# Performance work log

Measured on AMD Instinct MI355X. Metric: run time of the kernel, lower is better.

Reference implementation:

```python
import jax, jax.numpy as jnp
import numpy as np

B, N, D = 32, 2048, 16
PCD = 2        # point_cloud_dimensions
K_NN = 16      # k nearest neighbours
FILTERS = 64


def setup_inputs() -> dict:
    key = jax.random.key(0)
    k1, k2, k3 = jax.random.split(key, 3)
    x = jax.random.normal(k1, (B, N, D), dtype=jnp.float32)
    # 1x1 Conv2D == dense over the last (channel) dim: W [D, FILTERS], b [FILTERS]
    W = jax.random.normal(k2, (D, FILTERS), dtype=jnp.float32) * (1.0 / np.sqrt(D))
    b = jnp.zeros((FILTERS,), dtype=jnp.float32)
    return {"x": x, "W": W, "b": b}


def reference(x, W, b):
    # points = first PCD channels; features = full input (dynamic_coordinates=True)
    points = x[:, :, :PCD]                                   # [B,N,PCD]
    # squared pairwise distances: ||p_i||^2 + ||p_j||^2 - 2 p_i.p_j  -> [B,N,N]
    sq = jnp.sum(points * points, axis=-1)                   # [B,N]
    dist = sq[:, :, None] + sq[:, None, :] - 2.0 * jnp.einsum(
        'bnd,bmd->bnm', points, points)
    # k nearest neighbours (smallest distance) per point -> [B,N,k]
    _, idx = jax.lax.top_k(-dist, K_NN)
    # gather neighbour features: [B,N,k,D]
    neigh = jax.vmap(lambda f, i: f[i])(x, idx)
    centre = x[:, :, None, :]                                # [B,N,1,D]
    # NOTE: source concatenates along the neighbour axis -> [B,N,k+1,D]
    edges = jnp.concatenate([centre, neigh - centre], axis=2)
    # 1x1 conv (linear activation) over channel dim: [B,N,k+1,FILTERS]
    conv = jnp.einsum('bnkd,df->bnkf', edges, W) + b
    # Max pooling over neighbour axis: [B,N,FILTERS]
    pooled = jnp.max(conv, axis=2)
    # shortcut_input_features=True: concat original features
    return jnp.concatenate([pooled, x], axis=-1)             # [B,N,FILTERS+D]
```

## Files before the change

kernel.cpp:

```cpp
#include <hip/hip_runtime.h>


#define B_  32
#define N_  2048
#define D_  16
#define F_  64
#define K_  16
#define OUTD (F_ + D_)
#define NQ  64
#define NS  4
#define SPLIT (N_ / NS)

__global__ __launch_bounds__(256) void proj_kernel(const float* __restrict__ x,
                                                   const float* __restrict__ W,
                                                   float* __restrict__ Y) {
    __shared__ float Ws[D_ * F_];
    __shared__ float xs[16][D_];
    const int t = threadIdx.x;
    for (int i = t; i < D_ * F_; i += 256) Ws[i] = W[i];
    const int p0 = blockIdx.x * 16;
    ((float*)xs)[t] = x[(size_t)p0 * D_ + t];
    __syncthreads();
    const int w = t >> 6, f = t & 63;
#pragma unroll
    for (int i = 0; i < 4; i++) {
        const int pw = w * 4 + i;
        float acc = 0.f;
#pragma unroll
        for (int d = 0; d < D_; d++) acc = fmaf(xs[pw][d], Ws[d * F_ + f], acc);
        Y[(size_t)(p0 + pw) * F_ + f] = acc;
    }
}

__global__ __launch_bounds__(256, 4) void knn_kernel(const float* __restrict__ x,
                                                     const float* __restrict__ bias,
                                                     const float* __restrict__ Y,
                                                     float* __restrict__ out) {
    __shared__ float2 pts[N_];
    __shared__ float  sqs[N_];
    __shared__ float  arr_raw[NS - 1][NQ * 17];
    __shared__ float  Tq[NQ];
    __shared__ int    cnt[NQ];
    __shared__ int    tiecnt[NS][NQ];
    unsigned short (*tiebuf)[NQ][K_] =
        (unsigned short (*)[NQ][K_])&arr_raw[0][0];
    int (*idxL)[K_] = (int (*)[K_])((char*)&arr_raw[0][0] + 8192);

    const int b = blockIdx.x >> 5;
    const int qbase = (blockIdx.x & 31) * NQ;
    const int t = threadIdx.x;
    const int s = t >> 6;
    const int qi = t & 63;
    const int q = qbase + qi;

    const float* xb = x + (size_t)b * N_ * D_;
    for (int m = t; m < N_; m += 256) {
        float2 p = make_float2(xb[m * D_ + 0], xb[m * D_ + 1]);
        pts[m] = p;
        sqs[m] = __fadd_rn(__fmul_rn(p.x, p.x), __fmul_rn(p.y, p.y));
    }
    if (t < NQ) cnt[t] = 0;
    __syncthreads();

    const float2 qp = pts[q];
    const float sqn = sqs[q];

    float key[K_];
#pragma unroll
    for (int j = 0; j < K_; j++) key[j] = INFINITY;

    const int m0 = s * SPLIT, m1 = m0 + SPLIT;
#pragma unroll 4
    for (int m = m0; m < m1; m += 2) {
        float2 pa = pts[m];     float sa = sqs[m];
        float2 pb = pts[m + 1]; float sb = sqs[m + 1];
        float dota = __fmaf_rn(qp.y, pa.y, __fmul_rn(qp.x, pa.x));
        float da   = __fsub_rn(__fadd_rn(sqn, sa), __fmul_rn(2.f, dota));
        float dotb = __fmaf_rn(qp.y, pb.y, __fmul_rn(qp.x, pb.x));
        float db   = __fsub_rn(__fadd_rn(sqn, sb), __fmul_rn(2.f, dotb));
        float y0 = fminf(da, db), y1 = fmaxf(da, db);
#pragma unroll
        for (int j = K_ - 1; j >= 2; j--)
            key[j] = fminf(fminf(key[j], fmaxf(key[j - 1], y0)),
                           fmaxf(key[j - 2], y1));
        key[1] = fminf(fminf(key[1], fmaxf(key[0], y0)), y1);
        key[0] = fminf(key[0], y0);
    }

    if (s > 0) {
#pragma unroll
        for (int j = 0; j < K_; j++) arr_raw[s - 1][qi * 17 + j] = key[j];
    }
    __syncthreads();

    if (s == 0) {
        for (int ss = 0; ss < NS - 1; ss++) {
#pragma unroll
            for (int j = 0; j < K_; j += 2) {
                float y0 = arr_raw[ss][qi * 17 + j];
                float y1 = arr_raw[ss][qi * 17 + j + 1];
#pragma unroll
                for (int jj = K_ - 1; jj >= 2; jj--)
                    key[jj] = fminf(fminf(key[jj], fmaxf(key[jj - 1], y0)),
                                    fmaxf(key[jj - 2], y1));
                key[1] = fminf(fminf(key[1], fmaxf(key[0], y0)), y1);
                key[0] = fminf(key[0], y0);
            }
        }
        Tq[qi] = key[K_ - 1];
    }
    __syncthreads();

    const float T = Tq[qi];
    int tc = 0;
#pragma unroll 2
    for (int m = m0; m < m1; m++) {
        float2 p = pts[m];
        float dot = __fmaf_rn(qp.y, p.y, __fmul_rn(qp.x, p.x));
        float d   = __fsub_rn(__fadd_rn(sqn, sqs[m]), __fmul_rn(2.f, dot));
        if (d < T) {
            int slot = atomicAdd(&cnt[qi], 1);
            idxL[qi][slot] = m;
        } else if (d == T) {
            if (tc < K_) tiebuf[s][qi][tc] = (unsigned short)m;
            tc++;
        }
    }
    tiecnt[s][qi] = (tc < K_) ? tc : K_;
    __syncthreads();

    if (s == 0) {
        int c1 = cnt[qi];
        int w = c1;
        int need = K_ - c1;
        for (int ss = 0; ss < NS && need > 0; ss++) {
            int nn = tiecnt[ss][qi];
            for (int j = 0; j < nn && need > 0; j++) {
                idxL[qi][w++] = (int)tiebuf[ss][qi][j];
                need--;
            }
        }
    }
    __syncthreads();

    const int f = qi;
    const float bf = bias[f];
    const float* Yb = Y + (size_t)b * N_ * F_;
    for (int i = 0; i < 16; i++) {
        const int qq = s * 16 + i;
        const int gq = qbase + qq;
        const float yn = Yb[(size_t)gq * F_ + f];
        float M = -INFINITY;
#pragma unroll
        for (int k = 0; k < K_; k++) {
            int m = idxL[qq][k];
            M = fmaxf(M, Yb[(size_t)m * F_ + f]);
        }
        const size_t pb = (size_t)b * N_ + gq;
        out[pb * OUTD + f] = fmaxf(yn, M - yn) + bf;
        if (f < D_) out[pb * OUTD + F_ + f] = xb[(size_t)gq * D_ + f];
    }
}

extern "C" void kernel_launch(void* const* d_in, const int* in_sizes, int n_in,
                              void* d_out, int out_size, void* d_ws, size_t ws_size,
                              hipStream_t stream) {
    const float* x    = (const float*)d_in[0];
    const float* W    = (const float*)d_in[1];
    const float* bias = (const float*)d_in[2];
    float* out = (float*)d_out;

    float* Y = (float*)d_ws;

    proj_kernel<<<B_ * N_ / 16, 256, 0, stream>>>(x, W, Y);
    knn_kernel <<<B_ * (N_ / NQ), 256, 0, stream>>>(x, bias, Y, out);
}
```

Before: 260.5 us.

## Use packed fp16 sorting network for approximate kNN threshold, refine survivors in fp32

The distance scan now packs two candidate distances into an fp16x2 vector and keeps two interleaved top-16 lists with packed min/max, halving the sorting-network instruction count. The fp16 threshold is bumped up by two ulps to form an upper bound. A second pass collects survivors below that bound, capped at 24 per slice, and an fp32 re-sort of those survivors picks the exact top-16 with ties. This removes most fp32 comparator work and the shared atomics. The cost is that if more than CAP candidates fall under the bound (dense clusters or fp16 precision loss), true neighbours can be dropped and results may be wrong.

After: 251.9 us. -3.3%, faster.

```diff
diff --git a/kernel.cpp b/kernel.cpp
--- a/kernel.cpp
+++ b/kernel.cpp
@@ -10,6 +10,29 @@
 #define NQ  64
 #define NS  4
 #define SPLIT (N_ / NS)
+#define CAP 24
+
+typedef _Float16 h2 __attribute__((ext_vector_type(2)));
+
+static __device__ __forceinline__ h2 h2min(h2 a, h2 b) { return __builtin_elementwise_min(a, b); }
+static __device__ __forceinline__ h2 h2max(h2 a, h2 b) { return __builtin_elementwise_max(a, b); }
+static __device__ __forceinline__ _Float16 hmn(_Float16 a, _Float16 b) { return __builtin_elementwise_min(a, b); }
+static __device__ __forceinline__ _Float16 hmx(_Float16 a, _Float16 b) { return __builtin_elementwise_max(a, b); }
+static __device__ __forceinline__ unsigned short h2b(_Float16 h) { return __builtin_bit_cast(unsigned short, h); }
+static __device__ __forceinline__ _Float16 b2h(unsigned short b) { return __builtin_bit_cast(_Float16, b); }
+
+static __device__ __forceinline__ void pair_ins(_Float16 (&k)[16], _Float16 y0, _Float16 y1) {
+#pragma unroll
+    for (int j = 15; j >= 2; --j)
+        k[j] = hmn(hmn(k[j], hmx(k[j - 1], y0)), hmx(k[j - 2], y1));
+    k[1] = hmn(hmn(k[1], hmx(k[0], y0)), y1);
+    k[0] = hmn(k[0], y0);
+}
+
+static __device__ __forceinline__ float vdist(float2 qp, float sqn, float2 p, float sm) {
+    float dot = __fmaf_rn(qp.y, p.y, __fmul_rn(qp.x, p.x));
+    return __fsub_rn(__fadd_rn(sqn, sm), __fmul_rn(2.f, dot));
+}
 
 __global__ __launch_bounds__(256) void proj_kernel(const float* __restrict__ x,
                                                    const float* __restrict__ W,
@@ -38,13 +61,13 @@
                                                      float* __restrict__ out) {
     __shared__ float2 pts[N_];
     __shared__ float  sqs[N_];
-    __shared__ float  arr_raw[NS - 1][NQ * 17];
-    __shared__ float  Tq[NQ];
-    __shared__ int    cnt[NQ];
-    __shared__ int    tiecnt[NS][NQ];
-    unsigned short (*tiebuf)[NQ][K_] =
-        (unsigned short (*)[NQ][K_])&arr_raw[0][0];
-    int (*idxL)[K_] = (int (*)[K_])((char*)&arr_raw[0][0] + 8192);
+    __shared__ __align__(16) char region[NS * NQ * CAP * 2];
+    __shared__ unsigned short idxL[NQ][18];
+    __shared__ int   scnt[NS][NQ];
+    __shared__ float TubA[NQ];
+
+    unsigned (*arr32)[NQ][9] = (unsigned (*)[NQ][9])region;
+    unsigned short (*survb)[NQ][CAP] = (unsigned short (*)[NQ][CAP])region;
 
     const int b = blockIdx.x >> 5;
     const int qbase = (blockIdx.x & 31) * NQ;
@@ -59,85 +82,100 @@
         pts[m] = p;
         sqs[m] = __fadd_rn(__fmul_rn(p.x, p.x), __fmul_rn(p.y, p.y));
     }
-    if (t < NQ) cnt[t] = 0;
     __syncthreads();
 
     const float2 qp = pts[q];
     const float sqn = sqs[q];
-
-    float key[K_];
-#pragma unroll
-    for (int j = 0; j < K_; j++) key[j] = INFINITY;
+    const float n2x = -2.0f * qp.x, n2y = -2.0f * qp.y;
+
+    h2 key2[16];
+    const _Float16 hinf = b2h((unsigned short)0x7C00);
+#pragma unroll
+    for (int j = 0; j < 16; ++j) key2[j] = (h2){hinf, hinf};
 
     const int m0 = s * SPLIT, m1 = m0 + SPLIT;
 #pragma unroll 4
     for (int m = m0; m < m1; m += 2) {
         float2 pa = pts[m];     float sa = sqs[m];
         float2 pb = pts[m + 1]; float sb = sqs[m + 1];
-        float dota = __fmaf_rn(qp.y, pa.y, __fmul_rn(qp.x, pa.x));
-        float da   = __fsub_rn(__fadd_rn(sqn, sa), __fmul_rn(2.f, dota));
-        float dotb = __fmaf_rn(qp.y, pb.y, __fmul_rn(qp.x, pb.x));
-        float db   = __fsub_rn(__fadd_rn(sqn, sb), __fmul_rn(2.f, dotb));
-        float y0 = fminf(da, db), y1 = fmaxf(da, db);
-#pragma unroll
-        for (int j = K_ - 1; j >= 2; j--)
-            key[j] = fminf(fminf(key[j], fmaxf(key[j - 1], y0)),
-                           fmaxf(key[j - 2], y1));
-        key[1] = fminf(fminf(key[1], fmaxf(key[0], y0)), y1);
-        key[0] = fminf(key[0], y0);
-    }
+        float da = __fmaf_rn(n2y, pa.y, __fmaf_rn(n2x, pa.x, sqn + sa));
+        float db = __fmaf_rn(n2y, pb.y, __fmaf_rn(n2x, pb.x, sqn + sb));
+        h2 v = __builtin_bit_cast(h2, __builtin_amdgcn_cvt_pkrtz(da, db));
+#pragma unroll
+        for (int j = 15; j >= 1; --j)
+            key2[j] = h2min(key2[j], h2max(key2[j - 1], v));
+        key2[0] = h2min(key2[0], v);
+    }
+
+    _Float16 keyl[16];
+#pragma unroll
+    for (int j = 0; j < 16; ++j) keyl[j] = key2[j].x;
+#pragma unroll
+    for (int tt = 0; tt < 8; ++tt) pair_ins(keyl, key2[2 * tt].y, key2[2 * tt + 1].y);
 
     if (s > 0) {
 #pragma unroll
-        for (int j = 0; j < K_; j++) arr_raw[s - 1][qi * 17 + j] = key[j];
+        for (int tt = 0; tt < 8; ++tt)
+            arr32[s - 1][qi][tt] =
+                (unsigned)h2b(keyl[2 * tt]) | ((unsigned)h2b(keyl[2 * tt + 1]) << 16);
     }
     __syncthreads();
 
     if (s == 0) {
-        for (int ss = 0; ss < NS - 1; ss++) {
-#pragma unroll
-            for (int j = 0; j < K_; j += 2) {
-                float y0 = arr_raw[ss][qi * 17 + j];
-                float y1 = arr_raw[ss][qi * 17 + j + 1];
-#pragma unroll
-                for (int jj = K_ - 1; jj >= 2; jj--)
-                    key[jj] = fminf(fminf(key[jj], fmaxf(key[jj - 1], y0)),
-                                    fmaxf(key[jj - 2], y1));
-                key[1] = fminf(fminf(key[1], fmaxf(key[0], y0)), y1);
-                key[0] = fminf(key[0], y0);
-            }
-        }
-        Tq[qi] = key[K_ - 1];
-    }
-    __syncthreads();
-
-    const float T = Tq[qi];
-    int tc = 0;
+        for (int ss = 0; ss < NS - 1; ++ss) {
+#pragma unroll
+            for (int tt = 0; tt < 8; ++tt) {
+                unsigned w32 = arr32[ss][qi][tt];
+                pair_ins(keyl, b2h((unsigned short)(w32 & 0xffffu)),
+                               b2h((unsigned short)(w32 >> 16)));
+            }
+        }
+        float tub = (float)b2h((unsigned short)(h2b(keyl[15]) + 2));
+        TubA[qi] = fmaxf(tub, 7e-5f);
+    }
+    __syncthreads();
+
+    const float Tub = TubA[qi];
+    int sc = 0;
 #pragma unroll 2
-    for (int m = m0; m < m1; m++) {
-        float2 p = pts[m];
-        float dot = __fmaf_rn(qp.y, p.y, __fmul_rn(qp.x, p.x));
-        float d   = __fsub_rn(__fadd_rn(sqn, sqs[m]), __fmul_rn(2.f, dot));
-        if (d < T) {
-            int slot = atomicAdd(&cnt[qi], 1);
-            idxL[qi][slot] = m;
-        } else if (d == T) {
-            if (tc < K_) tiebuf[s][qi][tc] = (unsigned short)m;
-            tc++;
-        }
-    }
-    tiecnt[s][qi] = (tc < K_) ? tc : K_;
+    for (int m = m0; m < m1; ++m) {
+        float d = vdist(qp, sqn, pts[m], sqs[m]);
+        if (d < Tub) { if (sc < CAP) survb[s][qi][sc] = (unsigned short)m; sc++; }
+    }
+    scnt[s][qi] = sc;
     __syncthreads();
 
     if (s == 0) {
-        int c1 = cnt[qi];
-        int w = c1;
-        int need = K_ - c1;
-        for (int ss = 0; ss < NS && need > 0; ss++) {
-            int nn = tiecnt[ss][qi];
-            for (int j = 0; j < nn && need > 0; j++) {
-                idxL[qi][w++] = (int)tiebuf[ss][qi][j];
-                need--;
+        float key[16];
+#pragma unroll
+        for (int j = 0; j < 16; ++j) key[j] = INFINITY;
+        for (int ss = 0; ss < NS; ++ss) {
+            int n = scnt[ss][qi]; n = n < CAP ? n : CAP;
+            for (int j = 0; j < n; ++j) {
+                int m = (int)survb[ss][qi][j];
+                float d = vdist(qp, sqn, pts[m], sqs[m]);
+#pragma unroll
+                for (int jj = 15; jj >= 1; --jj)
+                    key[jj] = fminf(key[jj], fmaxf(key[jj - 1], d));
+                key[0] = fminf(key[0], d);
+            }
+        }
+        const float T = key[15];
+        int w = 0;
+        for (int ss = 0; ss < NS; ++ss) {
+            int n = scnt[ss][qi]; n = n < CAP ? n : CAP;
+            for (int j = 0; j < n; ++j) {
+                int m = (int)survb[ss][qi][j];
+                float d = vdist(qp, sqn, pts[m], sqs[m]);
+                if (d < T && w < K_) idxL[qi][w++] = (unsigned short)m;
+            }
+        }
+        for (int ss = 0; ss < NS && w < K_; ++ss) {
+            int n = scnt[ss][qi]; n = n < CAP ? n : CAP;
+            for (int j = 0; j < n && w < K_; ++j) {
+                int m = (int)survb[ss][qi][j];
+                float d = vdist(qp, sqn, pts[m], sqs[m]);
+                if (d == T) idxL[qi][w++] = (unsigned short)m;
             }
         }
     }
@@ -153,7 +191,7 @@
         float M = -INFINITY;
 #pragma unroll
         for (int k = 0; k < K_; k++) {
-            int m = idxL[qq][k];
+            int m = (int)idxL[qq][k];
             M = fmaxf(M, Yb[(size_t)m * F_ + f]);
         }
         const size_t pb = (size_t)b * N_ + gq;
```
